# Kernel optimization log

Measured on AMD Instinct MI355X. Metric: run time of the kernel, lower is better.

## Reference

```python
import jax, jax.numpy as jnp
import numpy as np

# dims: channels=512, kernel_size=1, stride=1
B, N, D = 8, 4096, 512
G, GC = 32, 16          # involution groups = D // 16, group_channels = 16
RED = D // 4            # involution reduction_ratio = 4
HID = int(D * 0.25) + 1 # CondConv attention hidden = int(in_planes*0.25)+1 = 129
K = 4                   # number of dynamic-conv experts
TEMP = 34.0             # CondConv softmax temperature
EPS = 1e-5


def setup_inputs() -> dict:
    key = jax.random.key(0)
    ks = jax.random.split(key, 6)
    sc = lambda k, shape, fan: jax.random.normal(k, shape, jnp.float32) / np.float32(np.sqrt(fan))
    return {
        "x": jax.random.normal(ks[0], (B, N, D), jnp.float32),
        # involution: 1x1 conv D->RED (no bias), eval-mode BN, 1x1 conv RED->G (k^2*groups with k=1)
        "conv1_w": sc(ks[1], (RED, D), D),
        "bn_gamma": jnp.ones((RED,), jnp.float32),
        "bn_beta": jnp.zeros((RED,), jnp.float32),
        "bn_mean": jnp.zeros((RED,), jnp.float32),
        "bn_var": jnp.ones((RED,), jnp.float32),
        "conv2_w": sc(ks[2], (G, RED), RED),
        "conv2_b": jnp.zeros((G,), jnp.float32),
        # Dynamic_conv1d (CondConv): attention MLP + K expert 1x1 kernels [K, out, in]
        "fc1_w": sc(ks[3], (HID, D), D),
        "fc2_w": sc(ks[4], (K, HID), HID),
        "fc2_b": jnp.zeros((K,), jnp.float32),
        "dyn_w": sc(ks[5], (K, D, D), D),
        "dyn_b": jnp.zeros((K, D), jnp.float32),
        # LayerNorm(channels)
        "ln_gamma": jnp.ones((D,), jnp.float32),
        "ln_beta": jnp.zeros((D,), jnp.float32),
    }


def reference(x, conv1_w, bn_gamma, bn_beta, bn_mean, bn_var, conv2_w, conv2_b,
              fc1_w, fc2_w, fc2_b, dyn_w, dyn_b, ln_gamma, ln_beta):
    b, n, d = x.shape
    # --- involution branch (k=1, stride=1): per-position, per-group scalar gating ---
    h = jnp.einsum('bnd,rd->bnr', x, conv1_w)                       # 1x1 conv
    h = (h - bn_mean) / jnp.sqrt(bn_var + EPS) * bn_gamma + bn_beta # eval BN
    h = jax.nn.relu(h)
    gate = jnp.einsum('bnr,gr->bng', h, conv2_w) + conv2_b          # [b,n,G] kernel weights (k^2=1)
    out1 = (x.reshape(b, n, G, GC) * gate[..., None]).reshape(b, n, d)
    # --- CondConv dynamic conv1d branch (k=1) ---
    pooled = x.mean(axis=1)                                          # adaptive avg pool over length -> [b,d]
    a = jax.nn.relu(pooled @ fc1_w.T)                                # [b,HID]
    att = jax.nn.softmax((a @ fc2_w.T + fc2_b) / TEMP, axis=-1)      # [b,K]
    Wb = jnp.einsum('bk,kod->bod', att, dyn_w)                       # per-sample kernel [b,d,d]
    bb = att @ dyn_b                                                 # [b,d]
    out2 = jnp.einsum('bnd,bod->bno', x, Wb) + bb[:, None, :]
    # --- LayerNorm + double residual ---
    y = out1 + out2
    mu = y.mean(-1, keepdims=True)
    var = y.var(-1, keepdims=True)
    y = (y - mu) / jnp.sqrt(var + EPS) * ln_gamma + ln_beta
    return y + x
```

## Files before the change

### kernel.cpp

```cpp
#include <hip/hip_runtime.h>

#define DI __device__ __forceinline__

typedef __bf16 bf8 __attribute__((ext_vector_type(8)));
typedef float f4 __attribute__((ext_vector_type(4)));
typedef unsigned short us4 __attribute__((ext_vector_type(4)));
typedef unsigned short us8 __attribute__((ext_vector_type(8)));

#define BB 8
#define NN 4096
#define DD 512
#define RED 128
#define GG 32
#define HID 129

DI float b2f(unsigned short u) {
    union { unsigned int i; float f; } c; c.i = ((unsigned int)u) << 16; return c.f;
}
DI unsigned short f2b(float f) {
    union { float f; unsigned int i; } c; c.f = f;
    unsigned int u = c.i;
    return (unsigned short)((u + 0x7fffu + ((u >> 16) & 1u)) >> 16);
}

typedef const __attribute__((address_space(1))) void* gp1_t;
typedef __attribute__((address_space(3))) void* lp3_t;
DI void gld16(const void* g, void* l) {
    __builtin_amdgcn_global_load_lds((gp1_t)g, (lp3_t)l, 16, 0, 0);
}

__global__ __launch_bounds__(256) void kpre(const float* __restrict__ x,
                                            const float* __restrict__ conv1_w,
                                            const float* __restrict__ conv2_w,
                                            float* __restrict__ part,
                                            unsigned short* __restrict__ xb,
                                            unsigned short* __restrict__ c1b,
                                            unsigned short* __restrict__ c2b) {
    int c = blockIdx.x, b = blockIdx.y, t = threadIdx.x;
    __shared__ float red[2][512];
    if (c >= 128) {
        int idx = ((c - 128) * 8 + b) * 256 + t;
        if (idx < 16384) {
            size_t off = (size_t)idx * 4;
            float4 v = *(const float4*)(conv1_w + off);
            us4 o; o[0] = f2b(v.x); o[1] = f2b(v.y); o[2] = f2b(v.z); o[3] = f2b(v.w);
            *(us4*)(c1b + off) = o;
        } else if (idx < 17408) {
            size_t off = (size_t)(idx - 16384) * 4;
            float4 v = *(const float4*)(conv2_w + off);
            us4 o; o[0] = f2b(v.x); o[1] = f2b(v.y); o[2] = f2b(v.z); o[3] = f2b(v.w);
            *(us4*)(c2b + off) = o;
        }
        return;
    }
    int rg = t >> 7, cg = t & 127;
    int row0 = c * 32 + rg * 16;
    float4 s = {0.f, 0.f, 0.f, 0.f};
#pragma unroll 4
    for (int i = 0; i < 16; ++i) {
        size_t off = ((size_t)(b * NN + row0 + i) * DD) + cg * 4;
        float4 v = *(const float4*)(x + off);
        s.x += v.x; s.y += v.y; s.z += v.z; s.w += v.w;
        us4 o; o[0] = f2b(v.x); o[1] = f2b(v.y); o[2] = f2b(v.z); o[3] = f2b(v.w);
        *(us4*)(xb + off) = o;
    }
    *(float4*)&red[rg][cg * 4] = s;
    __syncthreads();
    if (t < 128) {
        float4 aa = *(const float4*)&red[0][t * 4];
        float4 bb4 = *(const float4*)&red[1][t * 4];
        float4 o;
        o.x = aa.x + bb4.x; o.y = aa.y + bb4.y;
        o.z = aa.z + bb4.z; o.w = aa.w + bb4.w;
        *(float4*)(part + (size_t)(b * 128 + c) * DD + t * 4) = o;
    }
}

__global__ __launch_bounds__(256, 3) void kgate(
    const unsigned short* __restrict__ xb, const unsigned short* __restrict__ c1b,
    const float* __restrict__ bn_g, const float* __restrict__ bn_b,
    const float* __restrict__ bn_m, const float* __restrict__ bn_v,
    const unsigned short* __restrict__ c2b, const float* __restrict__ conv2_b,
    float* __restrict__ gate) {
    int bid = blockIdx.x;
    int b = bid & 7, mtile = bid >> 3;
    int row0 = mtile * 128;
    int t = threadIdx.x;
    int w = t >> 6, lane = t & 63, q = lane >> 4, l16 = lane & 15;
    int wr = (w & 1) * 64, wc = (w >> 1) * 64;
    int qa = (q ^ ((l16 >> 1) & 3)) * 8;

    __shared__ unsigned short As[4096], Bs[4096];
    __shared__ unsigned short h_s[128][136];
    __shared__ float bnS[RED], bnT[RED];

    if (t < RED) {
        float sc = bn_g[t] * rsqrtf(bn_v[t] + 1e-5f);
        bnS[t] = sc;
        bnT[t] = bn_b[t] - bn_m[t] * sc;
    }

    f4 acc[4][4];
#pragma unroll
    for (int mi = 0; mi < 4; ++mi)
#pragma unroll
        for (int ni = 0; ni < 4; ++ni) acc[mi][ni] = (f4){0.f, 0.f, 0.f, 0.f};

    const unsigned short* abase = xb + ((size_t)(b * NN + row0) * DD);
    const int r1 = t >> 2, k1 = (((t & 3) ^ ((t >> 3) & 3))) * 8;
    const int r2 = 64 + r1;
    unsigned short* As1 = &As[(size_t)w * 512];
    unsigned short* As2 = &As[2048 + (size_t)w * 512];
    unsigned short* Bs1 = &Bs[(size_t)w * 512];
    unsigned short* Bs2 = &Bs[2048 + (size_t)w * 512];

    for (int ks = 0; ks < 16; ++ks) {
        __syncthreads();
        int kk = ks * 32;
        gld16(abase + (size_t)r1 * DD + kk + k1, As1);
        gld16(abase + (size_t)r2 * DD + kk + k1, As2);
        gld16(c1b + (size_t)r1 * DD + kk + k1, Bs1);
        gld16(c1b + (size_t)r2 * DD + kk + k1, Bs2);
        __syncthreads();
        bf8 af[4], bv[4];
#pragma unroll
        for (int mi = 0; mi < 4; ++mi) af[mi] = *(const bf8*)&As[(wr + mi * 16 + l16) * 32 + qa];
#pragma unroll
        for (int ni = 0; ni < 4; ++ni) bv[ni] = *(const bf8*)&Bs[(wc + ni * 16 + l16) * 32 + qa];
#pragma unroll
        for (int ni = 0; ni < 4; ++ni)
#pragma unroll
            for (int mi = 0; mi < 4; ++mi)
                acc[mi][ni] = __builtin_amdgcn_mfma_f32_16x16x32_bf16(af[mi], bv[ni], acc[mi][ni], 0, 0, 0);
    }
    __syncthreads();
#pragma unroll
    for (int ni = 0; ni < 4; ++ni) {
        int hc = wc + ni * 16 + l16;
        float sc = bnS[hc], sh = bnT[hc];
#pragma unroll
        for (int mi = 0; mi < 4; ++mi)
#pragma unroll
            for (int r = 0; r < 4; ++r) {
                int row = wr + mi * 16 + q * 4 + r;
                h_s[row][hc] = f2b(fmaxf(acc[mi][ni][r] * sc + sh, 0.f));
            }
    }
    __syncthreads();
    f4 a2[2][2];
#pragma unroll
    for (int mi = 0; mi < 2; ++mi)
#pragma unroll
        for (int ni = 0; ni < 2; ++ni) a2[mi][ni] = (f4){0.f, 0.f, 0.f, 0.f};
#pragma unroll
    for (int ks = 0; ks < 4; ++ks) {
        bf8 ah[2], bh[2];
#pragma unroll
        for (int mi = 0; mi < 2; ++mi)
            ah[mi] = *(const bf8*)&h_s[w * 32 + mi * 16 + l16][ks * 32 + q * 8];
#pragma unroll
        for (int ni = 0; ni < 2; ++ni)
            bh[ni] = *(const bf8*)(c2b + (ni * 16 + l16) * RED + ks * 32 + q * 8);
#pragma unroll
        for (int ni = 0; ni < 2; ++ni)
#pragma unroll
            for (int mi = 0; mi < 2; ++mi)
                a2[mi][ni] = __builtin_amdgcn_mfma_f32_16x16x32_bf16(ah[mi], bh[ni], a2[mi][ni], 0, 0, 0);
    }
#pragma unroll
    for (int ni = 0; ni < 2; ++ni) {
        int g = ni * 16 + l16;
        float cb = conv2_b[g];
#pragma unroll
        for (int mi = 0; mi < 2; ++mi)
#pragma unroll
            for (int r = 0; r < 4; ++r) {
                int row = w * 32 + mi * 16 + q * 4 + r;
                gate[((size_t)(b * NN + row0 + row)) * GG + g] = a2[mi][ni][r] + cb;
            }
    }
}

__global__ __launch_bounds__(256) void katt(const float* __restrict__ part,
                                            const float* __restrict__ fc1_w,
                                            const float* __restrict__ fc2_w,
                                            const float* __restrict__ fc2_b,
                                            const float* __restrict__ dyn_b,
                                            float* __restrict__ att, float* __restrict__ bb) {
    int b = blockIdx.x, t = threadIdx.x;
    __shared__ float sh[2][512];
    __shared__ float pooled[512];
    __shared__ float a_s[HID + 3];
    __shared__ float att_s[4];
    {
        int cg = t & 127, half = t >> 7;
        const float* pb = part + ((size_t)b * 128 + half * 64) * DD + cg * 4;
        float4 s = {0.f, 0.f, 0.f, 0.f};
#pragma unroll 8
        for (int r = 0; r < 64; ++r) {
            float4 v = *(const float4*)(pb + (size_t)r * DD);
            s.x += v.x; s.y += v.y; s.z += v.z; s.w += v.w;
        }
        *(float4*)&sh[half][cg * 4] = s;
    }
    __syncthreads();
    if (t < 128) {
        float4 aa = *(const float4*)&sh[0][t * 4];
        float4 bb4 = *(const float4*)&sh[1][t * 4];
        float4 o;
        o.x = (aa.x + bb4.x) * (1.0f / (float)NN);
        o.y = (aa.y + bb4.y) * (1.0f / (float)NN);
        o.z = (aa.z + bb4.z) * (1.0f / (float)NN);
        o.w = (aa.w + bb4.w) * (1.0f / (float)NN);
        *(float4*)&pooled[t * 4] = o;
    }
    __syncthreads();
    int wv = t >> 6, ln = t & 63;
    float pl[8];
    {
        float4 p0 = *(const float4*)&pooled[ln * 8];
        float4 p1 = *(const float4*)&pooled[ln * 8 + 4];
        pl[0] = p0.x; pl[1] = p0.y; pl[2] = p0.z; pl[3] = p0.w;
        pl[4] = p1.x; pl[5] = p1.y; pl[6] = p1.z; pl[7] = p1.w;
    }
    for (int jb = wv * 4; jb < 128; jb += 16) {
        float s4[4];
#pragma unroll
        for (int u = 0; u < 4; ++u) {
            const float* wr = fc1_w + (size_t)(jb + u) * DD + ln * 8;
            float4 w0 = *(const float4*)wr;
            float4 w1 = *(const float4*)(wr + 4);
            s4[u] = w0.x * pl[0] + w0.y * pl[1] + w0.z * pl[2] + w0.w * pl[3] +
                    w1.x * pl[4] + w1.y * pl[5] + w1.z * pl[6] + w1.w * pl[7];
        }
#pragma unroll
        for (int u = 0; u < 4; ++u) {
            float v = s4[u];
#pragma unroll
            for (int off = 32; off >= 1; off >>= 1) v += __shfl_xor(v, off);
            if (ln == 0) a_s[jb + u] = fmaxf(v, 0.f);
        }
    }
    if (wv == 0) {
        const float* wr = fc1_w + (size_t)128 * DD + ln * 8;
        float4 w0 = *(const float4*)wr;
        float4 w1 = *(const float4*)(wr + 4);
        float v = w0.x * pl[0] + w0.y * pl[1] + w0.z * pl[2] + w0.w * pl[3] +
                  w1.x * pl[4] + w1.y * pl[5] + w1.z * pl[6] + w1.w * pl[7];
#pragma unroll
        for (int off = 32; off >= 1; off >>= 1) v += __shfl_xor(v, off);
        if (ln == 0) a_s[128] = fmaxf(v, 0.f);
    }
    __syncthreads();
    {
        float v = 0.f;
        for (int j = ln; j < HID; j += 64) v += a_s[j] * fc2_w[wv * HID + j];
#pragma unroll
        for (int off = 32; off >= 1; off >>= 1) v += __shfl_xor(v, off);
        if (ln == 0) att_s[wv] = (v + fc2_b[wv]) * (1.0f / 34.0f);
    }
    __syncthreads();
    if (t == 0) {
        float lg[4], mx = -1e30f;
#pragma unroll
        for (int k = 0; k < 4; ++k) { lg[k] = att_s[k]; mx = fmaxf(mx, lg[k]); }
        float den = 0.f;
#pragma unroll
        for (int k = 0; k < 4; ++k) { lg[k] = __expf(lg[k] - mx); den += lg[k]; }
#pragma unroll
        for (int k = 0; k < 4; ++k) {
            float a = lg[k] / den;
            att_s[k] = a; att[b * 4 + k] = a;
        }
    }
    __syncthreads();
    float a0 = att_s[0], a1 = att_s[1], a2 = att_s[2], a3 = att_s[3];
    for (int o = t; o < DD; o += 256) {
        bb[b * DD + o] = a0 * dyn_b[o] + a1 * dyn_b[DD + o] +
                         a2 * dyn_b[2 * DD + o] + a3 * dyn_b[3 * DD + o];
    }
}

__global__ __launch_bounds__(256) void kwb(const float* __restrict__ dyn_w,
                                           const float* __restrict__ att,
                                           unsigned short* __restrict__ Wb) {
    int g = blockIdx.x * 256 + threadIdx.x;
    size_t pos = (size_t)g * 4;
    float4 w0 = *(const float4*)(dyn_w + pos);
    float4 w1 = *(const float4*)(dyn_w + 262144 + pos);
    float4 w2 = *(const float4*)(dyn_w + 524288 + pos);
    float4 w3 = *(const float4*)(dyn_w + 786432 + pos);
#pragma unroll
    for (int b = 0; b < 8; ++b) {
        float a0 = att[b * 4 + 0], a1 = att[b * 4 + 1], a2 = att[b * 4 + 2], a3 = att[b * 4 + 3];
        us4 o;
        o[0] = f2b(a0 * w0.x + a1 * w1.x + a2 * w2.x + a3 * w3.x);
        o[1] = f2b(a0 * w0.y + a1 * w1.y + a2 * w2.y + a3 * w3.y);
        o[2] = f2b(a0 * w0.z + a1 * w1.z + a2 * w2.z + a3 * w3.z);
        o[3] = f2b(a0 * w0.w + a1 * w1.w + a2 * w2.w + a3 * w3.w);
        *(us4*)(Wb + (size_t)b * 262144 + pos) = o;
    }
}

#define STG_BUF 36864
#define XSTR 520
__global__ __launch_bounds__(512) void kfuse(
    const unsigned short* __restrict__ xb, const unsigned short* __restrict__ Wb,
    const float* __restrict__ bb, const float* __restrict__ gate,
    const float* __restrict__ lnG, const float* __restrict__ lnB,
    float* __restrict__ out) {
    int bid = blockIdx.x;
    int b = bid & 7, mtile = bid >> 3;
    int row0 = mtile * 64;
    int t = threadIdx.x;
    int w = t >> 6, lane = t & 63, q = lane >> 4, l16 = lane & 15;
    int wrow = (w >> 2) * 32, wcol = (w & 3) * 128;
    int qa = (q ^ ((l16 >> 1) & 3)) * 8;

    __shared__ __align__(16) char smem[73728];
    unsigned short* xs = (unsigned short*)smem;
    float2* redS = (float2*)(smem + 66560);
    float2* murs = (float2*)(smem + 68608);

    const unsigned short* abase = xb + ((size_t)(b * NN + row0) * DD);
    const unsigned short* wbase = Wb + ((size_t)b * DD) * DD;

    const int srow = lane >> 2, skoff = (((lane & 3) ^ ((lane >> 3) & 3))) * 8;

#define STAGE(bf, kk) do {                                                                  \
        unsigned short* Ab = (unsigned short*)(smem + (bf) * STG_BUF);                      \
        unsigned short* Bb = (unsigned short*)(smem + (bf) * STG_BUF + 4096);               \
        if (w < 4)                                                                          \
            gld16(abase + (size_t)(w * 16 + srow) * DD + (kk) + skoff, Ab + w * 512);       \
        _Pragma("unroll")                                                                   \
        for (int i_ = 0; i_ < 4; ++i_)                                                      \
            gld16(wbase + (size_t)((w * 4 + i_) * 16 + srow) * DD + (kk) + skoff,           \
                  Bb + (w * 4 + i_) * 512);                                                 \
    } while (0)

    f4 acc[2][8];
#pragma unroll
    for (int mi = 0; mi < 2; ++mi)
#pragma unroll
        for (int ni = 0; ni < 8; ++ni) acc[mi][ni] = (f4){0.f, 0.f, 0.f, 0.f};

    STAGE(0, 0);
    __syncthreads();
    for (int ks = 0; ks < 16; ++ks) {
        if (ks < 15) STAGE((ks + 1) & 1, (ks + 1) * 32);
        const unsigned short* A = (const unsigned short*)(smem + (ks & 1) * STG_BUF);
        const unsigned short* B = (const unsigned short*)(smem + (ks & 1) * STG_BUF + 4096);
        bf8 af[2], bv[8];
#pragma unroll
        for (int mi = 0; mi < 2; ++mi) af[mi] = *(const bf8*)&A[(wrow + mi * 16 + l16) * 32 + qa];
#pragma unroll
        for (int ni = 0; ni < 8; ++ni) bv[ni] = *(const bf8*)&B[(wcol + ni * 16 + l16) * 32 + qa];
#pragma unroll
        for (int ni = 0; ni < 8; ++ni)
#pragma unroll
            for (int mi = 0; mi < 2; ++mi)
                acc[mi][ni] = __builtin_amdgcn_mfma_f32_16x16x32_bf16(af[mi], bv[ni], acc[mi][ni], 0, 0, 0);
        __syncthreads();
    }

#pragma unroll
    for (int i = 0; i < 8; ++i) {
        int row = w * 8 + i;
        gld16(abase + (size_t)row * DD + lane * 8, xs + (size_t)row * XSTR);
    }
    float bbv[8], lgv[8], lbv[8];
#pragma unroll
    for (int ni = 0; ni < 8; ++ni) {
        int col = wcol + ni * 16 + l16;
        bbv[ni] = bb[b * DD + col];
        lgv[ni] = lnG[col];
        lbv[ni] = lnB[col];
    }
    __syncthreads();

    int g0 = wcol >> 4;
    const float* gbase = gate + ((size_t)(b * NN + row0)) * GG + g0;
#pragma unroll
    for (int mi = 0; mi < 2; ++mi) {
#pragma unroll
        for (int r = 0; r < 4; ++r) {
            int row = wrow + mi * 16 + q * 4 + r;
            float4 ga = *(const float4*)(gbase + (size_t)row * GG);
            float4 gb = *(const float4*)(gbase + (size_t)row * GG + 4);
            float gv[8] = {ga.x, ga.y, ga.z, ga.w, gb.x, gb.y, gb.z, gb.w};
            float s = 0.f, sq = 0.f;
#pragma unroll
            for (int ni = 0; ni < 8; ++ni) {
                int col = wcol + ni * 16 + l16;
                float xv = b2f(xs[(size_t)row * XSTR + col]);
                float y = acc[mi][ni][r] + bbv[ni] + xv * gv[ni];
                acc[mi][ni][r] = y;
                s += y; sq += y * y;
            }
#pragma unroll
            for (int off = 8; off >= 1; off >>= 1) {
                s += __shfl_xor(s, off);
                sq += __shfl_xor(sq, off);
            }
            if (l16 == 0) redS[row * 4 + (w & 3)] = make_float2(s, sq);
        }
    }
    __syncthreads();
    if (t < 64) {
        float2 r0 = redS[t * 4], r1 = redS[t * 4 + 1], r2 = redS[t * 4 + 2], r3 = redS[t * 4 + 3];
        float s = r0.x + r1.x + r2.x + r3.x;
        float sq = r0.y + r1.y + r2.y + r3.y;
        float mu = s * (1.f / 512.f);
        float rs = rsqrtf(sq * (1.f / 512.f) - mu * mu + 1e-5f);
        murs[t] = make_float2(mu, rs);
    }
    __syncthreads();
#pragma unroll
    for (int mi = 0; mi < 2; ++mi) {
#pragma unroll
        for (int r = 0; r < 4; ++r) {
            int row = wrow + mi * 16 + q * 4 + r;
            float2 mr = murs[row];
            float* op = out + ((size_t)(b * NN + row0 + row)) * DD;
#pragma unroll
            for (int ni = 0; ni < 8; ++ni) {
                int col = wcol + ni * 16 + l16;
                float xv = b2f(xs[(size_t)row * XSTR + col]);
                op[col] = (acc[mi][ni][r] - mr.x) * mr.y * lgv[ni] + lbv[ni] + xv;
            }
        }
    }
#undef STAGE
}

extern "C" void kernel_launch(void* const* d_in, const int* in_sizes, int n_in,
                              void* d_out, int out_size, void* d_ws, size_t ws_size,
                              hipStream_t stream) {
    const float* x       = (const float*)d_in[0];
    const float* conv1_w = (const float*)d_in[1];
    const float* bn_g    = (const float*)d_in[2];
    const float* bn_b    = (const float*)d_in[3];
    const float* bn_m    = (const float*)d_in[4];
    const float* bn_v    = (const float*)d_in[5];
    const float* conv2_w = (const float*)d_in[6];
    const float* conv2_b = (const float*)d_in[7];
    const float* fc1_w   = (const float*)d_in[8];
    const float* fc2_w   = (const float*)d_in[9];
    const float* fc2_b   = (const float*)d_in[10];
    const float* dyn_w   = (const float*)d_in[11];
    const float* dyn_b   = (const float*)d_in[12];
    const float* lnG     = (const float*)d_in[13];
    const float* lnB     = (const float*)d_in[14];
    float* out = (float*)d_out;

    char* ws = (char*)d_ws;
    unsigned short* xb   = (unsigned short*)ws;
    float* part          = (float*)(ws + 33554432);
    float* att           = (float*)(ws + 37748736);
    float* bbw           = (float*)(ws + 37748864);
    unsigned short* c1b  = (unsigned short*)(ws + 37765248);
    unsigned short* c2b  = (unsigned short*)(ws + 37896320);
    float* gate          = (float*)(ws + 37904512);
    unsigned short* Wb   = (unsigned short*)(ws + 42098816);

    kpre<<<dim3(137, 8), 256, 0, stream>>>(x, conv1_w, conv2_w, part, xb, c1b, c2b);
    kgate<<<256, 256, 0, stream>>>(xb, c1b, bn_g, bn_b, bn_m, bn_v, c2b, conv2_b, gate);
    katt<<<8, 256, 0, stream>>>(part, fc1_w, fc2_w, fc2_b, dyn_b, att, bbw);
    kwb<<<256, 256, 0, stream>>>(dyn_w, att, Wb);
    kfuse<<<512, 512, 0, stream>>>(xb, Wb, bbw, gate, lnG, lnB, out);
}
```

Measured before the change: 223.5 us.

## Double kfuse row tile and switch to triple-buffered async LDS pipeline

The fused GEMM+LayerNorm kernel now handles 128 rows per block instead of 64, so each wave holds a 4x8 accumulator tile and each staged slice of the per-sample weight matrix is reused across twice as many rows, with half as many blocks. The double-buffered staging loop becomes a three-stage ring that keeps two loads in flight, synchronized with explicit vmcnt waits and a single barrier per k-step. The aim is less redundant weight traffic and better hiding of load latency. In exchange it needs more registers and about 135KB of LDS, which leaves one block per CU and 256 blocks in total.

```diff
diff --git a/kernel.cpp b/kernel.cpp
--- a/kernel.cpp
+++ b/kernel.cpp
@@ -302,7 +302,8 @@
     }
 }
 
-#define STG_BUF 36864
+#define NBUF 3
+#define STG 40960
 #define XSTR 520
 __global__ __launch_bounds__(512) void kfuse(
     const unsigned short* __restrict__ xb, const unsigned short* __restrict__ Wb,
@@ -311,16 +312,16 @@
     float* __restrict__ out) {
     int bid = blockIdx.x;
     int b = bid & 7, mtile = bid >> 3;
-    int row0 = mtile * 64;
+    int row0 = mtile * 128;
     int t = threadIdx.x;
     int w = t >> 6, lane = t & 63, q = lane >> 4, l16 = lane & 15;
-    int wrow = (w >> 2) * 32, wcol = (w & 3) * 128;
+    int wrow = (w >> 2) * 64, wcol = (w & 3) * 128;
     int qa = (q ^ ((l16 >> 1) & 3)) * 8;
 
-    __shared__ __align__(16) char smem[73728];
+    __shared__ __align__(16) char smem[138240];
     unsigned short* xs = (unsigned short*)smem;
-    float2* redS = (float2*)(smem + 66560);
-    float2* murs = (float2*)(smem + 68608);
+    float2* redS = (float2*)(smem + 133120);
+    float2* murs = (float2*)(smem + 137216);
 
     const unsigned short* abase = xb + ((size_t)(b * NN + row0) * DD);
     const unsigned short* wbase = Wb + ((size_t)b * DD) * DD;
@@ -328,44 +329,51 @@
     const int srow = lane >> 2, skoff = (((lane & 3) ^ ((lane >> 3) & 3))) * 8;
 
 #define STAGE(bf, kk) do {                                                                  \
-        unsigned short* Ab = (unsigned short*)(smem + (bf) * STG_BUF);                      \
-        unsigned short* Bb = (unsigned short*)(smem + (bf) * STG_BUF + 4096);               \
-        if (w < 4)                                                                          \
-            gld16(abase + (size_t)(w * 16 + srow) * DD + (kk) + skoff, Ab + w * 512);       \
+        char* base_ = smem + (bf) * STG;                                                    \
         _Pragma("unroll")                                                                   \
-        for (int i_ = 0; i_ < 4; ++i_)                                                      \
-            gld16(wbase + (size_t)((w * 4 + i_) * 16 + srow) * DD + (kk) + skoff,           \
-                  Bb + (w * 4 + i_) * 512);                                                 \
+        for (int i_ = 0; i_ < 5; ++i_) {                                                    \
+            int cc_ = w * 5 + i_;                                                           \
+            if (cc_ < 8)                                                                    \
+                gld16(abase + (size_t)(cc_ * 16 + srow) * DD + (kk) + skoff,                \
+                      (unsigned short*)base_ + cc_ * 512);                                  \
+            else                                                                            \
+                gld16(wbase + (size_t)((cc_ - 8) * 16 + srow) * DD + (kk) + skoff,          \
+                      (unsigned short*)(base_ + 8192) + (cc_ - 8) * 512);                   \
+        }                                                                                   \
     } while (0)
 
-    f4 acc[2][8];
-#pragma unroll
-    for (int mi = 0; mi < 2; ++mi)
+    f4 acc[4][8];
+#pragma unroll
+    for (int mi = 0; mi < 4; ++mi)
 #pragma unroll
         for (int ni = 0; ni < 8; ++ni) acc[mi][ni] = (f4){0.f, 0.f, 0.f, 0.f};
 
     STAGE(0, 0);
-    __syncthreads();
+    STAGE(1, 32);
     for (int ks = 0; ks < 16; ++ks) {
-        if (ks < 15) STAGE((ks + 1) & 1, (ks + 1) * 32);
-        const unsigned short* A = (const unsigned short*)(smem + (ks & 1) * STG_BUF);
-        const unsigned short* B = (const unsigned short*)(smem + (ks & 1) * STG_BUF + 4096);
-        bf8 af[2], bv[8];
-#pragma unroll
-        for (int mi = 0; mi < 2; ++mi) af[mi] = *(const bf8*)&A[(wrow + mi * 16 + l16) * 32 + qa];
+        if (ks < 15) asm volatile("s_waitcnt vmcnt(5)" ::: "memory");
+        else         asm volatile("s_waitcnt vmcnt(0)" ::: "memory");
+        __builtin_amdgcn_s_barrier();
+        __builtin_amdgcn_sched_barrier(0);
+        if (ks + 2 < 16) STAGE((ks + 2) % NBUF, (ks + 2) * 32);
+        const unsigned short* A = (const unsigned short*)(smem + (ks % NBUF) * STG);
+        const unsigned short* B = (const unsigned short*)(smem + (ks % NBUF) * STG + 8192);
+        bf8 af[4], bv[8];
+#pragma unroll
+        for (int mi = 0; mi < 4; ++mi) af[mi] = *(const bf8*)&A[(wrow + mi * 16 + l16) * 32 + qa];
 #pragma unroll
         for (int ni = 0; ni < 8; ++ni) bv[ni] = *(const bf8*)&B[(wcol + ni * 16 + l16) * 32 + qa];
 #pragma unroll
         for (int ni = 0; ni < 8; ++ni)
 #pragma unroll
-            for (int mi = 0; mi < 2; ++mi)
+            for (int mi = 0; mi < 4; ++mi)
                 acc[mi][ni] = __builtin_amdgcn_mfma_f32_16x16x32_bf16(af[mi], bv[ni], acc[mi][ni], 0, 0, 0);
-        __syncthreads();
-    }
-
-#pragma unroll
-    for (int i = 0; i < 8; ++i) {
-        int row = w * 8 + i;
+    }
+    __syncthreads();
+
+#pragma unroll
+    for (int i = 0; i < 16; ++i) {
+        int row = w * 16 + i;
         gld16(abase + (size_t)row * DD + lane * 8, xs + (size_t)row * XSTR);
     }
     float bbv[8], lgv[8], lbv[8];
@@ -381,7 +389,7 @@
     int g0 = wcol >> 4;
     const float* gbase = gate + ((size_t)(b * NN + row0)) * GG + g0;
 #pragma unroll
-    for (int mi = 0; mi < 2; ++mi) {
+    for (int mi = 0; mi < 4; ++mi) {
 #pragma unroll
         for (int r = 0; r < 4; ++r) {
             int row = wrow + mi * 16 + q * 4 + r;
@@ -406,7 +414,7 @@
         }
     }
     __syncthreads();
-    if (t < 64) {
+    if (t < 128) {
         float2 r0 = redS[t * 4], r1 = redS[t * 4 + 1], r2 = redS[t * 4 + 2], r3 = redS[t * 4 + 3];
         float s = r0.x + r1.x + r2.x + r3.x;
         float sq = r0.y + r1.y + r2.y + r3.y;
@@ -416,7 +424,7 @@
     }
     __syncthreads();
 #pragma unroll
-    for (int mi = 0; mi < 2; ++mi) {
+    for (int mi = 0; mi < 4; ++mi) {
 #pragma unroll
         for (int r = 0; r < 4; ++r) {
             int row = wrow + mi * 16 + q * 4 + r;
@@ -467,5 +475,5 @@
     kgate<<<256, 256, 0, stream>>>(xb, c1b, bn_g, bn_b, bn_m, bn_v, c2b, conv2_b, gate);
     katt<<<8, 256, 0, stream>>>(part, fc1_w, fc2_w, fc2_b, dyn_b, att, bbw);
     kwb<<<256, 256, 0, stream>>>(dyn_w, att, Wb);
-    kfuse<<<512, 512, 0, stream>>>(xb, Wb, bbw, gate, lnG, lnB, out);
-}
+    kfuse<<<256, 512, 0, stream>>>(xb, Wb, bbw, gate, lnG, lnB, out);
+}
```

Measured after the change: 218.4 us. 1.02x faster.
